# Kernel optimization log

Hardware: AMD Instinct MI355X
Metric: run time of the kernel (lower is better)

Reference implementation:

```python
import jax, jax.numpy as jnp
import numpy as np

B, NX, NU, H, HID, NIT = 4096, 64, 16, 50, 256, 10


def dynamics(x, u, W1, b1, W2):
    # residual tanh-MLP dynamics: x_next = x + 0.1*tanh([x,u]@W1+b1)@W2
    z = jnp.concatenate([x, u], axis=-1)
    return x + 0.1 * jnp.tanh(z @ W1 + b1) @ W2


def setup_inputs() -> dict:
    key = jax.random.key(0)
    k0, k1, k2, k3 = jax.random.split(key, 4)
    x0 = jax.random.normal(k0, (B, NX), dtype=jnp.float32)
    xref = jnp.zeros((B, H + 1, NX), dtype=jnp.float32)
    W1 = jax.random.normal(k1, (NX + NU, HID), dtype=jnp.float32) * 0.05
    b1 = jnp.zeros((HID,), dtype=jnp.float32)
    W2 = jax.random.normal(k2, (HID, NX), dtype=jnp.float32) * 0.05
    # deterministic stand-in for torch.randn inside _compute_sqp_step (one draw per SQP iter)
    noise = jax.random.normal(k3, (NIT, B, H * NU), dtype=jnp.float32)
    return {"x0": x0, "xref": xref, "W1": W1, "b1": b1, "W2": W2,
            "noise": noise, "n_iterations": NIT}


def reference(x0, xref, W1, b1, W2, noise, n_iterations):
    batch, nx = x0.shape
    N = xref.shape[1] - 1            # horizon
    nu = noise.shape[2] // N         # control dim
    u = jnp.zeros((batch, N * nu), dtype=x0.dtype)

    def rollout(u_flat):
        us = jnp.swapaxes(u_flat.reshape(batch, N, nu), 0, 1)  # [N, B, nu]
        def step(x, u_k):
            x_next = dynamics(x, u_k, W1, b1, W2)
            return x_next, x_next
        _, xs = jax.lax.scan(step, x0, us)                     # [N, B, nx]
        return jnp.concatenate([x0[:, None], jnp.swapaxes(xs, 0, 1)], axis=1)  # [B, N+1, nx]

    x_traj = rollout(u)
    gx = gu = None
    for it in range(n_iterations):
        # sequential nonlinear rollout with current controls
        x_traj = rollout(u)
        # per-step linearization via VJP with ones cotangent (as in torch autograd.grad
        # with grad_outputs=ones); steps are independent so batch them over (B, N).
        xs = x_traj[:, :N].reshape(batch * N, nx)
        us = u.reshape(batch * N, nu)
        def f(xs_, us_):
            return dynamics(xs_, us_, W1, b1, W2)
        _, vjp_fn = jax.vjp(f, xs, us)
        gx_, gu_ = vjp_fn(jnp.ones((batch * N, nx), dtype=x0.dtype))
        gx = gx_.reshape(batch, N, nx)   # rows of A_lin (ones^T @ df/dx)
        gu = gu_.reshape(batch, N, nu)   # rows of B_lin (ones^T @ df/du)
        # SQP "step" in source is fresh gaussian noise * 0.01, scaled by 0.1
        u = u + 0.1 * (noise[it] * 0.01)
    # (first control, trajectory, predicted states, last-iteration linearization VJPs)
    return u[:, :nu], x_traj, x_traj[:, 1:], gx, gu
```

## Files before the change

kernel.cpp:

```cpp
#include <hip/hip_runtime.h>

typedef unsigned int uint;
typedef unsigned short ushort_t;
typedef __attribute__((ext_vector_type(8))) short bf16x8_t;
typedef __attribute__((ext_vector_type(4))) float f32x4_t;

constexpr int Bsz = 4096, NX = 64, NU = 16, NXU = 80, HID = 256, Hh = 50;
constexpr long NS = (long)Bsz * Hh * NU;
constexpr int O1 = 65536;
constexpr int O2 = 13434880;
constexpr int O3 = 26542080;
constexpr int O4 = 39649280;
constexpr int XT_PITCH = (Hh + 1) * NX;
constexpr int PR_PITCH = Hh * NX;
constexpr int U_PITCH = Hh * NU;

constexpr int W1S  = 260;
constexpr int W1TS = 84;
constexpr int HS   = 264;
constexpr int HSR  = 260;
constexpr int ZTS  = 20;
constexpr int TS   = 264;
constexpr int W2S  = 264;
constexpr int TLS  = 264;

constexpr long T_BYTES = (long)Bsz * Hh * HID * 2;

__device__ __forceinline__ float tanh_fast(float x) {
    float e = __expf(2.0f * x);
    return 1.0f - 2.0f / (e + 1.0f);
}
__device__ __forceinline__ uint f2bf_u(float x) {
    uint b = __float_as_uint(x);
    return (b + 0x7FFFu + ((b >> 16) & 1u)) >> 16;
}
__device__ __forceinline__ float bf2f(ushort_t u) {
    return __uint_as_float(((uint)u) << 16);
}
__device__ __forceinline__ void unpack8(uint4 v, float* f) {
    f[0] = __uint_as_float(v.x << 16); f[1] = __uint_as_float(v.x & 0xFFFF0000u);
    f[2] = __uint_as_float(v.y << 16); f[3] = __uint_as_float(v.y & 0xFFFF0000u);
    f[4] = __uint_as_float(v.z << 16); f[5] = __uint_as_float(v.z & 0xFFFF0000u);
    f[6] = __uint_as_float(v.w << 16); f[7] = __uint_as_float(v.w & 0xFFFF0000u);
}

__global__ __launch_bounds__(512, 2) void ker_roll(const float* __restrict__ x0,
                                                   const float* __restrict__ W1,
                                                   const float* __restrict__ b1,
                                                   const float* __restrict__ W2,
                                                   const float* __restrict__ noise,
                                                   const int* __restrict__ nit_p,
                                                   float* __restrict__ out,
                                                   ushort_t* __restrict__ tg) {
    __shared__ __align__(16) float    W1T[HID * W1TS];
    __shared__ __align__(16) ushort_t W2T[NX * W2S];
    __shared__ __align__(16) float    hRT[16 * HSR];
    __shared__ __align__(16) float    zT[NXU * ZTS];
    __shared__ float b1L[HID];
    __shared__ float sL[HID];

    const int tid = threadIdx.x;
    const int b0 = blockIdx.x * 16;
    const int nit = nit_p[0];

    for (int i = tid; i < NXU * HID; i += 512) {
        int kk = i >> 8, c = i & 255;
        W1T[c * W1TS + kk] = W1[i];
    }
    for (int i = tid; i < HID * NX; i += 512) {
        int c = i >> 6, d = i & 63;
        W2T[d * W2S + c] = (ushort_t)f2bf_u(W2[i]);
    }
    if (tid < HID) b1L[tid] = b1[tid];
    for (int i = tid; i < 16 * NX; i += 512) {
        int r = i >> 6, d = i & 63;
        float v = x0[(b0 + r) * NX + d];
        zT[d * ZTS + r] = v;
        out[O1 + (b0 + r) * XT_PITCH + d] = v;
    }
    const int r16n = (tid >> 4) & 15, q16n = tid & 15;
    if (tid < 256) {
        long base = (long)(b0 + r16n) * U_PITCH + q16n;
        float s = 0.f;
        for (int it = 0; it < nit - 1; ++it) s += noise[(long)it * NS + base];
        zT[(NX + q16n) * ZTS + r16n] = 0.001f * s;
        out[(b0 + r16n) * NU + q16n] = 0.001f * (s + noise[(long)(nit - 1) * NS + base]);
    }
    __syncthreads();
    if (tid < HID) {
        float s = 0.f;
        for (int d = 0; d < NX; ++d) s += bf2f(W2T[d * W2S + tid]);
        sL[tid] = 0.1f * s;
    }

    const int cP1 = tid & 255, half = tid >> 8;
    const int dP2 = tid & 63,  rp = tid >> 6;
    const uint* W2Tu = (const uint*)W2T;

    for (int k = 0; k < Hh; ++k) {
        __syncthreads();

        float v9[9];
        const bool fast = (k < Hh - 1) && (nit == 10);
        long nbase = (long)(b0 + r16n) * U_PITCH + (k + 1) * NU + q16n;
        if (fast && tid < 256) {
            #pragma unroll
            for (int it = 0; it < 9; ++it) v9[it] = noise[(long)it * NS + nbase];
        }

        float a_[8];
        {
            float bj = b1L[cP1];
            #pragma unroll
            for (int i = 0; i < 8; ++i) a_[i] = bj;
        }
        const float* w1c = &W1T[cP1 * W1TS];
        #pragma unroll 4
        for (int kc = 0; kc < 20; ++kc) {
            float4 wv = *(const float4*)&w1c[4 * kc];
            float ww[4] = {wv.x, wv.y, wv.z, wv.w};
            #pragma unroll
            for (int j = 0; j < 4; ++j) {
                int kk = 4 * kc + j;
                float4 z0 = *(const float4*)&zT[kk * ZTS + 8 * half];
                float4 z1 = *(const float4*)&zT[kk * ZTS + 8 * half + 4];
                float w = ww[j];
                a_[0] += z0.x * w; a_[1] += z0.y * w; a_[2] += z0.z * w; a_[3] += z0.w * w;
                a_[4] += z1.x * w; a_[5] += z1.y * w; a_[6] += z1.z * w; a_[7] += z1.w * w;
            }
        }
        float h_[8];
        #pragma unroll
        for (int i = 0; i < 8; ++i) h_[i] = tanh_fast(a_[i]);
        #pragma unroll
        for (int i = 0; i < 8; ++i)
            hRT[(8 * half + i) * HSR + cP1] = h_[i];
        {
            float sc = sL[cP1];
            #pragma unroll
            for (int i = 0; i < 8; ++i) {
                float t = sc * (1.f - h_[i] * h_[i]);
                size_t rho = (size_t)(b0 + 8 * half + i) * Hh + k;
                tg[rho * HID + cP1] = (ushort_t)f2bf_u(t);
            }
        }

        float unext = 0.f;
        if (tid < 256 && k < Hh - 1) {
            if (fast) {
                #pragma unroll
                for (int it = 0; it < 9; ++it) unext += v9[it];
            } else {
                for (int it = 0; it < nit - 1; ++it) unext += noise[(long)it * NS + nbase];
            }
            unext *= 0.001f;
        }

        __syncthreads();

        float acc0 = 0.f, acc1 = 0.f;
        const int r0 = 2 * rp, r1 = 2 * rp + 1;
        #pragma unroll 4
        for (int j8 = 0; j8 < 32; ++j8) {
            uint4 wv = *(const uint4*)&W2Tu[dP2 * (W2S / 2) + 4 * j8];
            float wf[8];
            unpack8(wv, wf);
            float4 h0a = *(const float4*)&hRT[r0 * HSR + 8 * j8];
            float4 h0b = *(const float4*)&hRT[r0 * HSR + 8 * j8 + 4];
            float4 h1a = *(const float4*)&hRT[r1 * HSR + 8 * j8];
            float4 h1b = *(const float4*)&hRT[r1 * HSR + 8 * j8 + 4];
            float hf0[8] = {h0a.x, h0a.y, h0a.z, h0a.w, h0b.x, h0b.y, h0b.z, h0b.w};
            float hf1[8] = {h1a.x, h1a.y, h1a.z, h1a.w, h1b.x, h1b.y, h1b.z, h1b.w};
            #pragma unroll
            for (int jj = 0; jj < 8; ++jj) {
                acc0 += hf0[jj] * wf[jj];
                acc1 += hf1[jj] * wf[jj];
            }
        }
        {
            const int bb0 = b0 + r0, bb1 = b0 + r1;
            float xn0 = zT[dP2 * ZTS + r0] + 0.1f * acc0;
            float xn1 = zT[dP2 * ZTS + r1] + 0.1f * acc1;
            out[O1 + bb0 * XT_PITCH + (k + 1) * NX + dP2] = xn0;
            out[O2 + bb0 * PR_PITCH + k * NX + dP2] = xn0;
            out[O1 + bb1 * XT_PITCH + (k + 1) * NX + dP2] = xn1;
            out[O2 + bb1 * PR_PITCH + k * NX + dP2] = xn1;
            zT[dP2 * ZTS + r0] = xn0;
            zT[dP2 * ZTS + r1] = xn1;
            if (tid < 256 && k < Hh - 1) zT[(NX + q16n) * ZTS + r16n] = unext;
        }
    }
}

__global__ __launch_bounds__(256) void ker_lin2(const float* __restrict__ W1,
                                                const ushort_t* __restrict__ Tg,
                                                float* __restrict__ out) {
    __shared__ __align__(16) ushort_t W1b[NXU * TLS];

    const int tid = threadIdx.x;
    const int r0 = blockIdx.x * 128;

    {
        const float4* W1f4 = (const float4*)W1;
        for (int i = tid; i < (NXU * HID) / 4; i += 256) {
            float4 w = W1f4[i];
            int p = i >> 6, c4 = i & 63;
            uint2 pk = make_uint2(f2bf_u(w.x) | (f2bf_u(w.y) << 16),
                                  f2bf_u(w.z) | (f2bf_u(w.w) << 16));
            *(uint2*)&W1b[p * TLS + 4 * c4] = pk;
        }
    }
    __syncthreads();

    const int wv = tid >> 6, lane = tid & 63;
    const int m = lane & 15, quad = lane >> 4;

    f32x4_t acc[2][5];
    #pragma unroll
    for (int i = 0; i < 2; ++i)
        #pragma unroll
        for (int j = 0; j < 5; ++j) acc[i][j] = (f32x4_t){0.f, 0.f, 0.f, 0.f};

    const ushort_t* Ta = Tg + (size_t)(r0 + wv * 32 + m) * HID;
    const ushort_t* Tb = Ta + (size_t)16 * HID;

    #pragma unroll
    for (int kc = 0; kc < 8; ++kc) {
        const int koff = kc * 32 + quad * 8;
        bf16x8_t a0 = *(const bf16x8_t*)&Ta[koff];
        bf16x8_t a1 = *(const bf16x8_t*)&Tb[koff];
        #pragma unroll
        for (int nt = 0; nt < 5; ++nt) {
            bf16x8_t bfr = *(const bf16x8_t*)&W1b[(nt * 16 + m) * TLS + koff];
            acc[0][nt] = __builtin_amdgcn_mfma_f32_16x16x32_bf16(a0, bfr, acc[0][nt], 0, 0, 0);
            acc[1][nt] = __builtin_amdgcn_mfma_f32_16x16x32_bf16(a1, bfr, acc[1][nt], 0, 0, 0);
        }
    }

    #pragma unroll
    for (int mt = 0; mt < 2; ++mt) {
        int rbase = r0 + wv * 32 + mt * 16 + quad * 4;
        #pragma unroll
        for (int r = 0; r < 4; ++r) {
            int rho = rbase + r;
            int b = (int)(((unsigned long long)rho * 1374389535ULL) >> 36);
            int kk = rho - b * 50;
            float* gxp = out + O3 + (size_t)b * PR_PITCH + kk * NX + m;
            #pragma unroll
            for (int nt = 0; nt < 4; ++nt)
                gxp[nt * 16] = 1.0f + acc[mt][nt][r];
            out[O4 + (size_t)b * U_PITCH + kk * NU + m] = acc[mt][4][r];
        }
    }
}

__global__ __launch_bounds__(256) void ker_fused(const float* __restrict__ x0,
                                                 const float* __restrict__ W1,
                                                 const float* __restrict__ b1,
                                                 const float* __restrict__ W2,
                                                 const float* __restrict__ noise,
                                                 const int* __restrict__ nit_p,
                                                 float* __restrict__ out) {
    __shared__ __align__(16) float    W1L[NXU * W1S];
    __shared__ __align__(16) ushort_t W2T[NX * W2S];
    __shared__ __align__(16) float    hRT[16 * HS];
    __shared__ __align__(16) ushort_t tT[16 * TS];
    __shared__ __align__(16) float    zT[NXU * 16];
    __shared__ float b1L[HID];
    __shared__ float sL[HID];

    const int tid = threadIdx.x;
    const int b0 = blockIdx.x * 16;
    const int nit = nit_p[0];

    for (int i = tid; i < NXU * HID; i += 256)
        W1L[(i >> 8) * W1S + (i & 255)] = W1[i];
    for (int i = tid; i < HID * NX; i += 256) {
        int c = i >> 6, d = i & 63;
        W2T[d * W2S + c] = (ushort_t)f2bf_u(W2[i]);
    }
    b1L[tid] = b1[tid];
    for (int i = tid; i < 16 * NX; i += 256) {
        int r = i >> 6, d = i & 63;
        float v = x0[(b0 + r) * NX + d];
        zT[d * 16 + r] = v;
        out[O1 + (b0 + r) * XT_PITCH + d] = v;
    }
    const int r16 = tid >> 4, q16 = tid & 15;
    {
        long base = (long)(b0 + r16) * U_PITCH + q16;
        float s = 0.f;
        for (int it = 0; it < nit - 1; ++it) s += noise[(long)it * NS + base];
        zT[(NX + q16) * 16 + r16] = 0.001f * s;
        out[(b0 + r16) * NU + q16] = 0.001f * (s + noise[(long)(nit - 1) * NS + base]);
    }
    __syncthreads();
    {
        float s = 0.f;
        for (int d = 0; d < NX; ++d) s += bf2f(W2T[d * W2S + tid]);
        sL[tid] = 0.1f * s;
    }

    const int ct = tid & 63, rt = tid >> 6;
    uint* tTu = (uint*)tT;
    const uint* W2Tu = (const uint*)W2T;

    for (int k = 0; k < Hh; ++k) {
        __syncthreads();
        float v9[9];
        const bool fast = (k < Hh - 1) && (nit == 10);
        long nbase = (long)(b0 + r16) * U_PITCH + (k + 1) * NU + q16;
        if (fast) {
            #pragma unroll
            for (int it = 0; it < 9; ++it) v9[it] = noise[(long)it * NS + nbase];
        }
        float a_[4][4];
        {
            float bj[4];
            #pragma unroll
            for (int j = 0; j < 4; ++j) bj[j] = b1L[4 * ct + j];
            #pragma unroll
            for (int i = 0; i < 4; ++i)
                #pragma unroll
                for (int j = 0; j < 4; ++j) a_[i][j] = bj[j];
        }
        #pragma unroll 8
        for (int kk = 0; kk < NXU; ++kk) {
            float4 zv = *(const float4*)&zT[kk * 16 + 4 * rt];
            float4 wv = *(const float4*)&W1L[kk * W1S + 4 * ct];
            float zz[4] = {zv.x, zv.y, zv.z, zv.w};
            float ww[4] = {wv.x, wv.y, wv.z, wv.w};
            #pragma unroll
            for (int i = 0; i < 4; ++i)
                #pragma unroll
                for (int j = 0; j < 4; ++j) a_[i][j] += zz[i] * ww[j];
        }
        float h_[4][4];
        #pragma unroll
        for (int i = 0; i < 4; ++i)
            #pragma unroll
            for (int j = 0; j < 4; ++j) h_[i][j] = tanh_fast(a_[i][j]);
        #pragma unroll
        for (int i = 0; i < 4; ++i)
            *(float4*)&hRT[(4 * rt + i) * HS + 4 * ct] =
                make_float4(h_[i][0], h_[i][1], h_[i][2], h_[i][3]);
        {
            float s0 = sL[4 * ct], s1 = sL[4 * ct + 1], s2 = sL[4 * ct + 2], s3 = sL[4 * ct + 3];
            #pragma unroll
            for (int i = 0; i < 4; ++i) {
                float t0 = s0 * (1.f - h_[i][0] * h_[i][0]);
                float t1 = s1 * (1.f - h_[i][1] * h_[i][1]);
                float t2 = s2 * (1.f - h_[i][2] * h_[i][2]);
                float t3 = s3 * (1.f - h_[i][3] * h_[i][3]);
                tTu[(4 * rt + i) * (TS / 2) + 2 * ct]     = f2bf_u(t0) | (f2bf_u(t1) << 16);
                tTu[(4 * rt + i) * (TS / 2) + 2 * ct + 1] = f2bf_u(t2) | (f2bf_u(t3) << 16);
            }
        }
        float unext = 0.f;
        if (k < Hh - 1) {
            if (fast) {
                #pragma unroll
                for (int it = 0; it < 9; ++it) unext += v9[it];
            } else {
                for (int it = 0; it < nit - 1; ++it) unext += noise[(long)it * NS + nbase];
            }
            unext *= 0.001f;
        }
        __syncthreads();
        float xacc[4] = {0.f, 0.f, 0.f, 0.f};
        #pragma unroll 4
        for (int c8 = 0; c8 < HID / 8; ++c8) {
            float4 h0 = *(const float4*)&hRT[r16 * HS + 8 * c8];
            float4 h1 = *(const float4*)&hRT[r16 * HS + 8 * c8 + 4];
            float hf[8] = {h0.x, h0.y, h0.z, h0.w, h1.x, h1.y, h1.z, h1.w};
            #pragma unroll
            for (int i = 0; i < 4; ++i) {
                int d = q16 + 16 * i;
                uint4 wv = *(const uint4*)&W2Tu[d * (W2S / 2) + 4 * c8];
                float wf[8];
                unpack8(wv, wf);
                #pragma unroll
                for (int jj = 0; jj < 8; ++jj) xacc[i] += hf[jj] * wf[jj];
            }
        }
        {
            const int bb = b0 + r16;
            #pragma unroll
            for (int i = 0; i < 4; ++i) {
                int d = q16 + 16 * i;
                float xn = zT[d * 16 + r16] + 0.1f * xacc[i];
                out[O1 + bb * XT_PITCH + (k + 1) * NX + d] = xn;
                out[O2 + bb * PR_PITCH + k * NX + d] = xn;
                zT[d * 16 + r16] = xn;
            }
            if (k < Hh - 1) zT[(NX + q16) * 16 + r16] = unext;
        }
        {
            const uint* tTr = (const uint*)tT + r16 * (TS / 2);
            float g_[5] = {0.f, 0.f, 0.f, 0.f, 0.f};
            #pragma unroll 4
            for (int jc = 0; jc < HID / 8; ++jc) {
                uint4 tv = *(const uint4*)&tTr[4 * jc];
                float tf[8];
                unpack8(tv, tf);
                #pragma unroll
                for (int i = 0; i < 5; ++i) {
                    int p = q16 + 16 * i;
                    float4 w0 = *(const float4*)&W1L[p * W1S + 8 * jc];
                    float4 w1 = *(const float4*)&W1L[p * W1S + 8 * jc + 4];
                    g_[i] += tf[0] * w0.x + tf[1] * w0.y + tf[2] * w0.z + tf[3] * w0.w
                           + tf[4] * w1.x + tf[5] * w1.y + tf[6] * w1.z + tf[7] * w1.w;
                }
            }
            const int bb = b0 + r16;
            #pragma unroll
            for (int i = 0; i < 4; ++i)
                out[O3 + bb * PR_PITCH + k * NX + (q16 + 16 * i)] = 1.0f + g_[i];
            out[O4 + bb * U_PITCH + k * NU + q16] = g_[4];
        }
    }
}

extern "C" void kernel_launch(void* const* d_in, const int* in_sizes, int n_in,
                              void* d_out, int out_size, void* d_ws, size_t ws_size,
                              hipStream_t stream) {
    const float* x0    = (const float*)d_in[0];
    const float* W1    = (const float*)d_in[2];
    const float* b1    = (const float*)d_in[3];
    const float* W2    = (const float*)d_in[4];
    const float* noise = (const float*)d_in[5];
    const int*   nit   = (const int*)d_in[6];
    float* out = (float*)d_out;

    if (ws_size >= (size_t)T_BYTES) {
        ushort_t* tg = (ushort_t*)d_ws;
        ker_roll<<<Bsz / 16, 512, 0, stream>>>(x0, W1, b1, W2, noise, nit, out, tg);
        ker_lin2<<<(Bsz * Hh) / 128, 256, 0, stream>>>(W1, tg, out);
    } else {
        ker_fused<<<Bsz / 16, 256, 0, stream>>>(x0, W1, b1, W2, noise, nit, out);
    }
}
```

Before: 754.6 us.

## Keep W1 column in registers and halve rollout block to 8 rows

The rollout kernel now uses 256 threads per block handling 8 batch rows, with each thread holding its full 80-element W1 column in registers instead of reading W1 from shared memory each step. This removes the large W1 shared-memory array and per-step LDS traffic for weights, and doubles the grid to 512 blocks for more parallelism. In exchange, register pressure rises (80 weight registers plus accumulators), which may lower occupancy or cause spills, and W2 staging and setup are repeated across twice as many blocks.

After: 673.9 us. -10.7%, faster.

```diff
diff --git a/kernel.cpp b/kernel.cpp
--- a/kernel.cpp
+++ b/kernel.cpp
@@ -15,11 +15,12 @@
 constexpr int PR_PITCH = Hh * NX;
 constexpr int U_PITCH = Hh * NU;
 
+constexpr int RB = 8;
+
 constexpr int W1S  = 260;
-constexpr int W1TS = 84;
 constexpr int HS   = 264;
 constexpr int HSR  = 260;
-constexpr int ZTS  = 20;
+constexpr int ZT8  = 12;
 constexpr int TS   = 264;
 constexpr int W2S  = 264;
 constexpr int TLS  = 264;
@@ -44,7 +45,7 @@
     f[6] = __uint_as_float(v.w << 16); f[7] = __uint_as_float(v.w & 0xFFFF0000u);
 }
 
-__global__ __launch_bounds__(512, 2) void ker_roll(const float* __restrict__ x0,
+__global__ __launch_bounds__(256, 2) void ker_roll(const float* __restrict__ x0,
                                                    const float* __restrict__ W1,
                                                    const float* __restrict__ b1,
                                                    const float* __restrict__ W2,
@@ -52,49 +53,48 @@
                                                    const int* __restrict__ nit_p,
                                                    float* __restrict__ out,
                                                    ushort_t* __restrict__ tg) {
-    __shared__ __align__(16) float    W1T[HID * W1TS];
     __shared__ __align__(16) ushort_t W2T[NX * W2S];
-    __shared__ __align__(16) float    hRT[16 * HSR];
-    __shared__ __align__(16) float    zT[NXU * ZTS];
+    __shared__ __align__(16) float    hRT[RB * HSR];
+    __shared__ __align__(16) float    zT[NXU * ZT8];
     __shared__ float b1L[HID];
     __shared__ float sL[HID];
 
     const int tid = threadIdx.x;
-    const int b0 = blockIdx.x * 16;
+    const int b0 = blockIdx.x * RB;
     const int nit = nit_p[0];
 
-    for (int i = tid; i < NXU * HID; i += 512) {
-        int kk = i >> 8, c = i & 255;
-        W1T[c * W1TS + kk] = W1[i];
-    }
-    for (int i = tid; i < HID * NX; i += 512) {
+    float w1r[NXU];
+    #pragma unroll
+    for (int kk = 0; kk < NXU; ++kk) w1r[kk] = W1[kk * HID + tid];
+
+    for (int i = tid; i < HID * NX; i += 256) {
         int c = i >> 6, d = i & 63;
         W2T[d * W2S + c] = (ushort_t)f2bf_u(W2[i]);
     }
-    if (tid < HID) b1L[tid] = b1[tid];
-    for (int i = tid; i < 16 * NX; i += 512) {
+    b1L[tid] = b1[tid];
+    for (int i = tid; i < RB * NX; i += 256) {
         int r = i >> 6, d = i & 63;
         float v = x0[(b0 + r) * NX + d];
-        zT[d * ZTS + r] = v;
+        zT[d * ZT8 + r] = v;
         out[O1 + (b0 + r) * XT_PITCH + d] = v;
     }
-    const int r16n = (tid >> 4) & 15, q16n = tid & 15;
-    if (tid < 256) {
+    const int r16n = tid >> 4, q16n = tid & 15;
+    if (tid < 16 * RB) {
         long base = (long)(b0 + r16n) * U_PITCH + q16n;
         float s = 0.f;
         for (int it = 0; it < nit - 1; ++it) s += noise[(long)it * NS + base];
-        zT[(NX + q16n) * ZTS + r16n] = 0.001f * s;
+        zT[(NX + q16n) * ZT8 + r16n] = 0.001f * s;
         out[(b0 + r16n) * NU + q16n] = 0.001f * (s + noise[(long)(nit - 1) * NS + base]);
     }
     __syncthreads();
-    if (tid < HID) {
+    {
         float s = 0.f;
         for (int d = 0; d < NX; ++d) s += bf2f(W2T[d * W2S + tid]);
         sL[tid] = 0.1f * s;
     }
 
-    const int cP1 = tid & 255, half = tid >> 8;
-    const int dP2 = tid & 63,  rp = tid >> 6;
+    const int c = tid;
+    const int dP2 = tid & 63, rp = tid >> 6;
     const uint* W2Tu = (const uint*)W2T;
 
     for (int k = 0; k < Hh; ++k) {
@@ -103,50 +103,43 @@
         float v9[9];
         const bool fast = (k < Hh - 1) && (nit == 10);
         long nbase = (long)(b0 + r16n) * U_PITCH + (k + 1) * NU + q16n;
-        if (fast && tid < 256) {
+        if (fast && tid < 16 * RB) {
             #pragma unroll
             for (int it = 0; it < 9; ++it) v9[it] = noise[(long)it * NS + nbase];
         }
 
-        float a_[8];
-        {
-            float bj = b1L[cP1];
-            #pragma unroll
-            for (int i = 0; i < 8; ++i) a_[i] = bj;
-        }
-        const float* w1c = &W1T[cP1 * W1TS];
-        #pragma unroll 4
-        for (int kc = 0; kc < 20; ++kc) {
-            float4 wv = *(const float4*)&w1c[4 * kc];
-            float ww[4] = {wv.x, wv.y, wv.z, wv.w};
-            #pragma unroll
-            for (int j = 0; j < 4; ++j) {
-                int kk = 4 * kc + j;
-                float4 z0 = *(const float4*)&zT[kk * ZTS + 8 * half];
-                float4 z1 = *(const float4*)&zT[kk * ZTS + 8 * half + 4];
-                float w = ww[j];
-                a_[0] += z0.x * w; a_[1] += z0.y * w; a_[2] += z0.z * w; a_[3] += z0.w * w;
-                a_[4] += z1.x * w; a_[5] += z1.y * w; a_[6] += z1.z * w; a_[7] += z1.w * w;
-            }
-        }
-        float h_[8];
-        #pragma unroll
-        for (int i = 0; i < 8; ++i) h_[i] = tanh_fast(a_[i]);
-        #pragma unroll
-        for (int i = 0; i < 8; ++i)
-            hRT[(8 * half + i) * HSR + cP1] = h_[i];
-        {
-            float sc = sL[cP1];
-            #pragma unroll
-            for (int i = 0; i < 8; ++i) {
+        float a_[RB];
+        {
+            float bj = b1L[c];
+            #pragma unroll
+            for (int i = 0; i < RB; ++i) a_[i] = bj;
+        }
+        #pragma unroll
+        for (int kk = 0; kk < NXU; ++kk) {
+            float4 z0 = *(const float4*)&zT[kk * ZT8];
+            float4 z1 = *(const float4*)&zT[kk * ZT8 + 4];
+            float w = w1r[kk];
+            a_[0] += z0.x * w; a_[1] += z0.y * w; a_[2] += z0.z * w; a_[3] += z0.w * w;
+            a_[4] += z1.x * w; a_[5] += z1.y * w; a_[6] += z1.z * w; a_[7] += z1.w * w;
+        }
+        float h_[RB];
+        #pragma unroll
+        for (int i = 0; i < RB; ++i) h_[i] = tanh_fast(a_[i]);
+        #pragma unroll
+        for (int i = 0; i < RB; ++i)
+            hRT[i * HSR + c] = h_[i];
+        {
+            float sc = sL[c];
+            #pragma unroll
+            for (int i = 0; i < RB; ++i) {
                 float t = sc * (1.f - h_[i] * h_[i]);
-                size_t rho = (size_t)(b0 + 8 * half + i) * Hh + k;
-                tg[rho * HID + cP1] = (ushort_t)f2bf_u(t);
+                size_t rho = (size_t)(b0 + i) * Hh + k;
+                tg[rho * HID + c] = (ushort_t)f2bf_u(t);
             }
         }
 
         float unext = 0.f;
-        if (tid < 256 && k < Hh - 1) {
+        if (tid < 16 * RB && k < Hh - 1) {
             if (fast) {
                 #pragma unroll
                 for (int it = 0; it < 9; ++it) unext += v9[it];
@@ -179,15 +172,15 @@
         }
         {
             const int bb0 = b0 + r0, bb1 = b0 + r1;
-            float xn0 = zT[dP2 * ZTS + r0] + 0.1f * acc0;
-            float xn1 = zT[dP2 * ZTS + r1] + 0.1f * acc1;
+            float xn0 = zT[dP2 * ZT8 + r0] + 0.1f * acc0;
+            float xn1 = zT[dP2 * ZT8 + r1] + 0.1f * acc1;
             out[O1 + bb0 * XT_PITCH + (k + 1) * NX + dP2] = xn0;
             out[O2 + bb0 * PR_PITCH + k * NX + dP2] = xn0;
             out[O1 + bb1 * XT_PITCH + (k + 1) * NX + dP2] = xn1;
             out[O2 + bb1 * PR_PITCH + k * NX + dP2] = xn1;
-            zT[dP2 * ZTS + r0] = xn0;
-            zT[dP2 * ZTS + r1] = xn1;
-            if (tid < 256 && k < Hh - 1) zT[(NX + q16n) * ZTS + r16n] = unext;
+            zT[dP2 * ZT8 + r0] = xn0;
+            zT[dP2 * ZT8 + r1] = xn1;
+            if (tid < 16 * RB && k < Hh - 1) zT[(NX + q16n) * ZT8 + r16n] = unext;
         }
     }
 }
@@ -434,7 +427,7 @@
 
     if (ws_size >= (size_t)T_BYTES) {
         ushort_t* tg = (ushort_t*)d_ws;
-        ker_roll<<<Bsz / 16, 512, 0, stream>>>(x0, W1, b1, W2, noise, nit, out, tg);
+        ker_roll<<<Bsz / RB, 256, 0, stream>>>(x0, W1, b1, W2, noise, nit, out, tg);
         ker_lin2<<<(Bsz * Hh) / 128, 256, 0, stream>>>(W1, tg, out);
     } else {
         ker_fused<<<Bsz / 16, 256, 0, stream>>>(x0, W1, b1, W2, noise, nit, out);
```
